# Optimization experiments

Hardware: AMD Instinct MI355X
Metric: run time of the kernel (lower is better)

The kernel has to match this reference:

```python
import jax, jax.numpy as jnp
import numpy as np

B, S, D, H = 2, 2048, 1024, 16
DH = D // H  # dim_per_head = 64


def setup_inputs() -> dict:
    key = jax.random.key(0)
    ks = jax.random.split(key, 12)
    std = 1.0 / np.sqrt(D)
    inp = {
        "key": jax.random.normal(ks[0], (B, S, D), jnp.float32),
        "value": jax.random.normal(ks[1], (B, S, D), jnp.float32),
        "query": jax.random.normal(ks[2], (B, S, D), jnp.float32),
        "mask": jax.random.randint(ks[3], (B, S, S), 0, 2) == 1,
        "Wk": jax.random.normal(ks[4], (D, D), jnp.float32) * std,
        "bk": jnp.zeros((D,), jnp.float32),
        "Wv": jax.random.normal(ks[5], (D, D), jnp.float32) * std,
        "bv": jnp.zeros((D,), jnp.float32),
        "Wq": jax.random.normal(ks[6], (D, D), jnp.float32) * std,
        "bq": jnp.zeros((D,), jnp.float32),
        "Wo": jax.random.normal(ks[7], (D, D), jnp.float32) * std,
        "bo": jnp.zeros((D,), jnp.float32),
    }
    return inp


def _shape(x):
    # (B, L, D) -> (B, H, L, DH)
    return x.reshape(B, -1, H, DH).transpose(0, 2, 1, 3)


def reference(key, value, query, mask, Wk, bk, Wv, bv, Wq, bq, Wo, bo):
    k = _shape(key @ Wk.T + bk)      # (B,H,S,DH)
    v = _shape(value @ Wv.T + bv)    # (B,H,S,DH)
    q = _shape(query @ Wq.T + bq)    # (B,H,S,DH)
    q = q / jnp.sqrt(jnp.asarray(DH, q.dtype))
    scores = jnp.einsum("bhqd,bhkd->bhqk", q, k).astype(jnp.float32)
    scores = jnp.where(mask[:, None, :, :], jnp.float32(-1e18), scores)
    attn = jax.nn.softmax(scores, axis=-1).astype(q.dtype)  # (B,H,S,S)
    # dropout p=0.0 -> identity
    ctx = jnp.einsum("bhqk,bhkd->bhqd", attn, v)
    ctx = ctx.transpose(0, 2, 1, 3).reshape(B, -1, D)
    output = ctx @ Wo.T + bo
    top_attn = attn[:, 0, :, :]
    return output, top_attn
```

## Files before the change

kernel.cpp:

```cpp
#include <hip/hip_runtime.h>

constexpr int BB = 2, SS = 2048, DD = 1024, HH = 16, DHH = 64;

typedef __attribute__((ext_vector_type(4))) float f32x4;
typedef __attribute__((ext_vector_type(8))) __bf16 bf16x8;
typedef __attribute__((ext_vector_type(8))) unsigned short us8;

__device__ __forceinline__ unsigned short f32_to_bf16(float f) {
    unsigned int u = __float_as_uint(f);
    u += 0x7fffu + ((u >> 16) & 1u);
    return (unsigned short)(u >> 16);
}

__device__ __forceinline__ ushort2 pk_bf16(float a, float b) {
#if __has_builtin(__builtin_amdgcn_cvt_pk_bf16_f32)
    typedef __attribute__((ext_vector_type(2))) __bf16 bf16x2;
    bf16x2 r = __builtin_amdgcn_cvt_pk_bf16_f32(a, b);
    return *(ushort2*)&r;
#else
    ushort2 r; r.x = f32_to_bf16(a); r.y = f32_to_bf16(b); return r;
#endif
}
__device__ __forceinline__ ushort4 pk_bf16x4(float a, float b, float c, float d) {
    const ushort2 lo = pk_bf16(a, b), hi = pk_bf16(c, d);
    ushort4 r; r.x = lo.x; r.y = lo.y; r.z = hi.x; r.w = hi.y;
    return r;
}

__device__ __forceinline__ f32x4 mfma_bf16(bf16x8 a, bf16x8 b, f32x4 c) {
    return __builtin_amdgcn_mfma_f32_16x16x32_bf16(a, b, c, 0, 0, 0);
}

__device__ __forceinline__ void stage16(const void* g, void* l) {
    typedef const __attribute__((address_space(1))) unsigned int gas_t;
    typedef __attribute__((address_space(3))) unsigned int las_t;
    __builtin_amdgcn_global_load_lds((gas_t*)(unsigned long long)g,
                                     (las_t*)(unsigned int)(unsigned long long)l,
                                     16, 0, 0);
}

__device__ __forceinline__ void cvt_block(const float* __restrict__ src,
                                          unsigned short* __restrict__ dst, int blk) {
    const size_t i = ((size_t)blk * 256 + threadIdx.x) * 8;
    const float4 a = *(const float4*)(src + i);
    const float4 b = *(const float4*)(src + i + 4);
    ushort4 lo = pk_bf16x4(a.x, a.y, a.z, a.w);
    ushort4 hi = pk_bf16x4(b.x, b.y, b.z, b.w);
    us8 o;
    o[0] = lo.x; o[1] = lo.y; o[2] = lo.z; o[3] = lo.w;
    o[4] = hi.x; o[5] = hi.y; o[6] = hi.z; o[7] = hi.w;
    *(us8*)(dst + i) = o;
}

__global__ __launch_bounds__(256) void cvt_bf16(const float* __restrict__ src,
                                                unsigned short* __restrict__ dst) {
    cvt_block(src, dst, blockIdx.x);
}

__global__ __launch_bounds__(256) void prep(const float* __restrict__ q,
                                            const float* __restrict__ k,
                                            const float* __restrict__ v,
                                            const float* __restrict__ Wq,
                                            const float* __restrict__ Wk,
                                            const float* __restrict__ Wv,
                                            unsigned short* __restrict__ Xq,
                                            unsigned short* __restrict__ Xk,
                                            unsigned short* __restrict__ Xv,
                                            unsigned short* __restrict__ Wqb,
                                            unsigned short* __restrict__ Wkb,
                                            unsigned short* __restrict__ Wvb,
                                            const int* __restrict__ mask,
                                            unsigned long long* __restrict__ pm) {
    const int id = blockIdx.x;
    if (id < 6144) {
        const int sel = id >> 11, blk = id & 2047;
        cvt_block(sel == 0 ? q : (sel == 1 ? k : v),
                  sel == 0 ? Xq : (sel == 1 ? Xk : Xv), blk);
    } else if (id < 7680) {
        const int wid = id - 6144;
        const int sel = wid >> 9, blk = wid & 511;
        cvt_block(sel == 0 ? Wq : (sel == 1 ? Wk : Wv),
                  sel == 0 ? Wqb : (sel == 1 ? Wkb : Wvb), blk);
    } else {
        const int mid = id - 7680;
        const int t = threadIdx.x, lane = t & 63;
#pragma unroll
        for (int it = 0; it < 4; ++it) {
            const size_t chunk = (size_t)mid * 16 + it * 4 + (t >> 6);
            const int val = mask[chunk * 64 + lane];
            const unsigned long long b = __ballot(val != 0);
            if (lane == 0) pm[chunk] = b;
        }
    }
}

__device__ __forceinline__ void gemm_body(int mode,
                                          const unsigned short* __restrict__ A,
                                          const unsigned short* __restrict__ Wb,
                                          const float* __restrict__ bias,
                                          void* __restrict__ outp,
                                          float scale, int nid,
                                          unsigned short* __restrict__ h0) {
    constexpr int K = DD;
    __shared__ __align__(16) unsigned short Ash[2][128][64];
    __shared__ __align__(16) unsigned short Bsh[2][64][64];

    const int n0 = (nid & 15) * 64;
    const int m0 = (nid >> 4) * 128;

    const int t = threadIdx.x;
    const int lane = t & 63, w = t >> 6;
    const int l15 = lane & 15, quad = lane >> 4;
    const int wm = (w >> 1) * 64, wn = (w & 1) * 32;

    const int srow = lane >> 3;
    const int scol8 = ((lane & 7) ^ srow) * 8;
    const unsigned short* Ag = A + (size_t)(m0 + w * 32 + srow) * K + scol8;
    const unsigned short* Bg = Wb + (size_t)(n0 + w * 16 + srow) * K + scol8;

    f32x4 acc[4][2] = {};

#pragma unroll
    for (int j = 0; j < 4; ++j) stage16(Ag + (size_t)j * 8 * K, &Ash[0][w * 32 + j * 8][0]);
#pragma unroll
    for (int j = 0; j < 2; ++j) stage16(Bg + (size_t)j * 8 * K, &Bsh[0][w * 16 + j * 8][0]);

    for (int kk = 0; kk < K / 64; ++kk) {
        const int cur = kk & 1;
        if (kk < K / 64 - 1) {
            const size_t ko = (size_t)(kk + 1) * 64;
#pragma unroll
            for (int j = 0; j < 4; ++j)
                stage16(Ag + (size_t)j * 8 * K + ko, &Ash[cur ^ 1][w * 32 + j * 8][0]);
#pragma unroll
            for (int j = 0; j < 2; ++j)
                stage16(Bg + (size_t)j * 8 * K + ko, &Bsh[cur ^ 1][w * 16 + j * 8][0]);
            __asm__ volatile("s_waitcnt vmcnt(6)" ::: "memory");
        } else {
            __asm__ volatile("s_waitcnt vmcnt(0)" ::: "memory");
        }
        __builtin_amdgcn_s_barrier();
        __builtin_amdgcn_sched_barrier(0);

        const unsigned short* Ab = &Ash[cur][0][0];
        const unsigned short* Bb = &Bsh[cur][0][0];

#pragma unroll
        for (int s = 0; s < 2; ++s) {
            const int ch = ((s * 4 + quad) ^ (l15 & 7)) * 8;
            bf16x8 af[4], bfr[2];
#pragma unroll
            for (int mi = 0; mi < 4; ++mi)
                af[mi] = *(const bf16x8*)&Ab[(wm + mi * 16 + l15) * 64 + ch];
#pragma unroll
            for (int ni = 0; ni < 2; ++ni)
                bfr[ni] = *(const bf16x8*)&Bb[(wn + ni * 16 + l15) * 64 + ch];
            __builtin_amdgcn_s_setprio(1);
#pragma unroll
            for (int mi = 0; mi < 4; ++mi)
#pragma unroll
                for (int ni = 0; ni < 2; ++ni)
                    acc[mi][ni] = mfma_bf16(af[mi], bfr[ni], acc[mi][ni]);
            __builtin_amdgcn_s_setprio(0);
        }
        __builtin_amdgcn_sched_barrier(0);
        __builtin_amdgcn_s_barrier();
        __builtin_amdgcn_sched_barrier(0);
    }

#pragma unroll
    for (int ni = 0; ni < 2; ++ni) {
        const int c = n0 + wn + ni * 16 + l15;
        const float bs = bias[c];
#pragma unroll
        for (int mi = 0; mi < 4; ++mi) {
#pragma unroll
            for (int r = 0; r < 4; ++r) {
                const int mrow = m0 + wm + mi * 16 + quad * 4 + r;
                const float val = (acc[mi][ni][r] + bs) * scale;
                if (mode == 2) {
                    ((float*)outp)[(size_t)mrow * DD + c] = val;
                } else {
                    const int bi2 = mrow >> 11, si = mrow & (SS - 1);
                    const int hi2 = c >> 6, di = c & (DHH - 1);
                    unsigned short* o = (unsigned short*)outp;
                    const unsigned short v16 = f32_to_bf16(val);
                    if (mode == 0) {
                        o[((size_t)(bi2 * HH + hi2) * SS + si) * DHH + di] = v16;
                        if (h0 != nullptr && hi2 == 0)
                            h0[((size_t)bi2 * SS + si) * DHH + di] = v16;
                    } else {
                        o[((size_t)(bi2 * HH + hi2) * DHH + di) * SS + si] = v16;
                    }
                }
            }
        }
    }
}

__global__ __launch_bounds__(256) void gemm_qv(const unsigned short* __restrict__ Xq,
                                               const unsigned short* __restrict__ Wqb,
                                               const float* __restrict__ bq,
                                               unsigned short* __restrict__ qws,
                                               float qscale,
                                               unsigned short* __restrict__ q0,
                                               const unsigned short* __restrict__ Xv,
                                               const unsigned short* __restrict__ Wvb,
                                               const float* __restrict__ bv,
                                               unsigned short* __restrict__ vws) {
    const int id = blockIdx.x;
    const int gid = id >> 9, id9 = id & 511;
    const int nid = (id9 & 7) * 64 + (id9 >> 3);
    gemm_body(gid, gid ? Xv : Xq, gid ? Wvb : Wqb, gid ? bv : bq,
              gid ? (void*)vws : (void*)qws, gid ? 1.0f : qscale, nid,
              gid ? nullptr : q0);
}

template <int MODE>
__global__ __launch_bounds__(256) void gemm_one(const unsigned short* __restrict__ A,
                                                const unsigned short* __restrict__ Wb,
                                                const float* __restrict__ bias,
                                                void* __restrict__ outp,
                                                float scale,
                                                unsigned short* __restrict__ h0) {
    const int id = blockIdx.x;
    const int nid = (id & 7) * 64 + (id >> 3);
    gemm_body(MODE, A, Wb, bias, outp, scale, nid, h0);
}

__global__ __launch_bounds__(512, 4) void flash_attn(const unsigned short* __restrict__ qws,
                                                     const unsigned short* __restrict__ kws,
                                                     const unsigned short* __restrict__ vws,
                                                     const unsigned long long* __restrict__ pm,
                                                     unsigned short* __restrict__ ctx,
                                                     float2* __restrict__ stats) {
    __shared__ __align__(16) unsigned short Ksh[2][64][64];
    __shared__ __align__(16) unsigned short Vsh[2][64][64];
    __shared__ __align__(16) unsigned short Psh[8][16][72];

    constexpr int NQT = SS / 128;
    const int id = blockIdx.x;
    const int nid = (id & 7) * 64 + (id >> 3);
    const int qt = nid % NQT;
    const int bh = nid / NQT;
    const int bi = bh / HH, hi = bh % HH;

    const int t = threadIdx.x;
    const int lane = t & 63, w = t >> 6;
    const int l15 = lane & 15, quad = lane >> 4;
    const int sh4 = quad * 4;
    const int xk = quad ^ (l15 & 7);

    const unsigned short* qp = qws + (size_t)bh * SS * DHH;
    const unsigned short* kp = kws + (size_t)bh * SS * DHH;
    const unsigned short* vp = vws + (size_t)bh * DHH * SS;

    const int q_loc = qt * 128 + w * 16 + l15;
    const bf16x8 bq0 = *(const bf16x8*)(qp + (size_t)q_loc * DHH + quad * 8);
    const bf16x8 bq1 = *(const bf16x8*)(qp + (size_t)q_loc * DHH + 32 + quad * 8);
    const unsigned long long* pmrow = pm + ((size_t)bi * SS + q_loc) * (SS / 64);

    const int srow = lane >> 3;
    const int scol = (lane & 7) ^ srow;
    const unsigned short* kg = kp + (size_t)(w * 8 + srow) * DHH + scol * 8;
    const unsigned short* vg = vp + (size_t)(w * 8 + srow) * SS + scol * 8;

    f32x4 accO[4] = {};
    float m_run = -1e30f, l_run = 0.f;
    const float NEG_INF = -__builtin_inff();

    unsigned long long mcur = pmrow[0];
    stage16(kg, &Ksh[0][w * 8][0]);
    stage16(vg, &Vsh[0][w * 8][0]);

    constexpr int NT = SS / 64;
    for (int kt = 0; kt < NT; ++kt) {
        const int cur = kt & 1;
        unsigned long long mnxt = 0;
        if (kt < NT - 1) {
            mnxt = pmrow[kt + 1];
            stage16(kg + (size_t)(kt + 1) * 64 * DHH, &Ksh[cur ^ 1][w * 8][0]);
            stage16(vg + (size_t)(kt + 1) * 64,       &Vsh[cur ^ 1][w * 8][0]);
            __asm__ volatile("s_waitcnt vmcnt(3)" ::: "memory");
        } else {
            __asm__ volatile("s_waitcnt vmcnt(0)" ::: "memory");
        }
        __builtin_amdgcn_s_barrier();
        __builtin_amdgcn_sched_barrier(0);

        const unsigned short* Kb = &Ksh[cur][0][0];
        const unsigned short* Vb = &Vsh[cur][0][0];

        bf16x8 ak0[4], ak1[4];
#pragma unroll
        for (int i = 0; i < 4; ++i) {
            ak0[i] = *(const bf16x8*)&Kb[(i * 16 + l15) * 64 + xk * 8];
            ak1[i] = *(const bf16x8*)&Kb[(i * 16 + l15) * 64 + (xk ^ 4) * 8];
        }

        const unsigned int mlo = ((unsigned int)mcur) >> sh4;
        const unsigned int mhi = ((unsigned int)(mcur >> 32)) >> sh4;

        float sc[4][4];
        __builtin_amdgcn_s_setprio(1);
#pragma unroll
        for (int i = 0; i < 4; ++i) {
            f32x4 s4 = {};
            s4 = mfma_bf16(ak0[i], bq0, s4);
            s4 = mfma_bf16(ak1[i], bq1, s4);
            const unsigned int mw = (i & 2) ? mhi : mlo;
#pragma unroll
            for (int r = 0; r < 4; ++r)
                sc[i][r] = ((mw >> ((i & 1) * 16 + r)) & 1u) ? NEG_INF : s4[r];
        }
        __builtin_amdgcn_s_setprio(0);

        bf16x8 av0[4], av1[4];
#pragma unroll
        for (int i = 0; i < 4; ++i) {
            av0[i] = *(const bf16x8*)&Vb[(i * 16 + l15) * 64 + xk * 8];
            av1[i] = *(const bf16x8*)&Vb[(i * 16 + l15) * 64 + (xk ^ 4) * 8];
        }

        float tm = sc[0][0];
#pragma unroll
        for (int i = 0; i < 4; ++i)
#pragma unroll
            for (int r = 0; r < 4; ++r) tm = fmaxf(tm, sc[i][r]);
        tm = fmaxf(tm, __shfl_xor(tm, 16));
        tm = fmaxf(tm, __shfl_xor(tm, 32));

        const bool nodefer = !__all(tm <= m_run + 8.0f);
        const float mn = nodefer ? fmaxf(m_run, tm) : m_run;

        float rs = 0.f;
#pragma unroll
        for (int i = 0; i < 4; ++i)
#pragma unroll
            for (int r = 0; r < 4; ++r) {
                const float p = __builtin_amdgcn_exp2f(sc[i][r] - mn);
                sc[i][r] = p;
                rs += p;
            }
        rs += __shfl_xor(rs, 16);
        rs += __shfl_xor(rs, 32);

        if (nodefer) {
            const float alpha = __builtin_amdgcn_exp2f(m_run - mn);
            l_run = l_run * alpha + rs;
            m_run = mn;
#pragma unroll
            for (int i = 0; i < 4; ++i) accO[i] *= alpha;
        } else {
            l_run += rs;
        }

#pragma unroll
        for (int i = 0; i < 4; ++i)
            *(ushort4*)&Psh[w][l15][i * 16 + sh4] =
                pk_bf16x4(sc[i][0], sc[i][1], sc[i][2], sc[i][3]);
        __asm__ volatile("s_waitcnt lgkmcnt(0)" ::: "memory");

        const bf16x8 p0 = *(const bf16x8*)&Psh[w][l15][quad * 8];
        const bf16x8 p1 = *(const bf16x8*)&Psh[w][l15][32 + quad * 8];
        __builtin_amdgcn_s_setprio(1);
#pragma unroll
        for (int i = 0; i < 4; ++i) {
            accO[i] = mfma_bf16(av0[i], p0, accO[i]);
            accO[i] = mfma_bf16(av1[i], p1, accO[i]);
        }
        __builtin_amdgcn_s_setprio(0);

        __builtin_amdgcn_sched_barrier(0);
        __builtin_amdgcn_s_barrier();
        __builtin_amdgcn_sched_barrier(0);
        mcur = mnxt;
    }

    const float inv = 1.0f / l_run;
    unsigned short* cb = ctx + ((size_t)(bi * SS) + q_loc) * DD + hi * DHH;
#pragma unroll
    for (int i = 0; i < 4; ++i)
        *(ushort4*)&cb[i * 16 + sh4] = pk_bf16x4(accO[i][0] * inv, accO[i][1] * inv,
                                                 accO[i][2] * inv, accO[i][3] * inv);

    if (hi == 0 && quad == 0) {
        float2 st; st.x = m_run; st.y = l_run;
        stats[(size_t)bi * SS + q_loc] = st;
    }
}

__global__ __launch_bounds__(256) void prob_h0(const unsigned short* __restrict__ q0,
                                               const unsigned short* __restrict__ k0,
                                               const unsigned long long* __restrict__ pm,
                                               const float2* __restrict__ stats,
                                               float* __restrict__ outp) {
    __shared__ __align__(16) unsigned short Ksh[64][72];

    const int id = blockIdx.x;
    const int nid = (id & 7) * 64 + (id >> 3);
    const int kc = nid & 7;
    const int qt = (nid >> 3) & 31;
    const int bi = nid >> 8;

    const int t = threadIdx.x;
    const int lane = t & 63, w = t >> 6;
    const int l15 = lane & 15, quad = lane >> 4;
    const int sh4 = quad * 4;

    const int q = qt * 64 + w * 16 + l15;
    const unsigned short* qp = q0 + ((size_t)bi * SS + q) * DHH;
    const bf16x8 bq0 = *(const bf16x8*)(qp + quad * 8);
    const bf16x8 bq1 = *(const bf16x8*)(qp + 32 + quad * 8);

    const unsigned short* kp = k0 + (size_t)bi * SS * DHH;
    const unsigned long long* pmq = pm + ((size_t)bi * SS + q) * (SS / 64);
    float* orow = outp + ((size_t)bi * SS + q) * SS;

    const float2 st = stats[(size_t)bi * SS + q];
    const float M = st.x;
    const float invL = 1.0f / st.y;

    for (int kt = 0; kt < 4; ++kt) {
        const int key0 = kc * 256 + kt * 64;
        __syncthreads();
#pragma unroll
        for (int hf = 0; hf < 2; ++hf) {
            const int v = t + hf * 256;
            const int row = v >> 3, off = (v & 7) * 8;
            *(us8*)&Ksh[row][off] = *(const us8*)(kp + (size_t)(key0 + row) * DHH + off);
        }
        __syncthreads();

        const unsigned long long m64 = pmq[kc * 4 + kt];
        const unsigned int mlo = ((unsigned int)m64) >> sh4;
        const unsigned int mhi = ((unsigned int)(m64 >> 32)) >> sh4;

#pragma unroll
        for (int i = 0; i < 4; ++i) {
            const bf16x8 ak0 = *(const bf16x8*)&Ksh[i * 16 + l15][quad * 8];
            const bf16x8 ak1 = *(const bf16x8*)&Ksh[i * 16 + l15][32 + quad * 8];
            f32x4 s4 = {};
            s4 = mfma_bf16(ak0, bq0, s4);
            s4 = mfma_bf16(ak1, bq1, s4);
            const unsigned int mw = (i & 2) ? mhi : mlo;
            float4 ov;
#pragma unroll
            for (int r = 0; r < 4; ++r) {
                const float p = __builtin_amdgcn_exp2f(s4[r] - M) * invL;
                ((float*)&ov)[r] = ((mw >> ((i & 1) * 16 + r)) & 1u) ? 0.0f : p;
            }
            *(float4*)&orow[key0 + i * 16 + sh4] = ov;
        }
    }
}

extern "C" void kernel_launch(void* const* d_in, const int* in_sizes, int n_in,
                              void* d_out, int out_size, void* d_ws, size_t ws_size,
                              hipStream_t stream) {
    const float* key_   = (const float*)d_in[0];
    const float* value_ = (const float*)d_in[1];
    const float* query_ = (const float*)d_in[2];
    const int*   mask_  = (const int*)d_in[3];
    const float* Wk = (const float*)d_in[4];
    const float* bk = (const float*)d_in[5];
    const float* Wv = (const float*)d_in[6];
    const float* bv = (const float*)d_in[7];
    const float* Wq = (const float*)d_in[8];
    const float* bq = (const float*)d_in[9];
    const float* Wo = (const float*)d_in[10];
    const float* bo = (const float*)d_in[11];

    constexpr size_t XS  = (size_t)BB * SS * DD;
    constexpr size_t WSZ = (size_t)DD * DD;

    float* out_f = (float*)d_out;
    unsigned short* scratch = (unsigned short*)(out_f + XS);
    unsigned short* qws = scratch;
    unsigned short* kws = qws + XS;
    unsigned short* vws = kws + XS;
    unsigned short* ctx = vws + XS;

    unsigned short* q0 = (unsigned short*)d_ws;
    unsigned short* k0 = q0 + (size_t)BB * SS * DHH;
    unsigned long long* pm = (unsigned long long*)(k0 + (size_t)BB * SS * DHH);
    float2* stats = (float2*)(pm + (size_t)BB * SS * (SS / 64));

    unsigned short* Xq  = (unsigned short*)out_f;
    unsigned short* Xk  = Xq + XS;
    unsigned short* Xv  = kws;
    unsigned short* Wqb = ctx;
    unsigned short* Wkb = Wqb + WSZ;
    unsigned short* Wvb = Wkb + WSZ;
    unsigned short* Wob = qws;

    const float qscale = 0.125f * 1.4426950408889634f;

    prep<<<15872, 256, 0, stream>>>(query_, key_, value_, Wq, Wk, Wv,
                                    Xq, Xk, Xv, Wqb, Wkb, Wvb, mask_, pm);

    gemm_qv<<<1024, 256, 0, stream>>>(Xq, Wqb, bq, qws, qscale, q0,
                                      Xv, Wvb, bv, vws);

    gemm_one<0><<<512, 256, 0, stream>>>(Xk, Wkb, bk, kws, 1.0f, k0);

    flash_attn<<<BB * HH * (SS / 128), 512, 0, stream>>>(qws, kws, vws, pm, ctx, stats);

    cvt_bf16<<<WSZ / 2048, 256, 0, stream>>>(Wo, Wob);

    gemm_one<2><<<512, 256, 0, stream>>>(ctx, Wob, bo, out_f, 1.0f, nullptr);

    prob_h0<<<512, 256, 0, stream>>>(q0, k0, pm, stats, out_f + XS);
}
```

Measured before the change: 302.9 us.

## Fuse Q/K/V projections into one 128x128-tile GEMM, fusing V fp32 conversion

Replaces the separate Q+V and K projection launches with one gemm_qkv kernel that uses 512-thread blocks and 128x128 output tiles. The V path reads fp32 value directly, converts it to bf16 in registers and writes it into swizzled LDS, so V no longer needs a pre-conversion pass in prep. The transposed V output is staged through LDS so it can be written with vectorized stores. The output projection also moves to a 128x128 tile with 512 threads, which halves the block count and increases reuse per block, at the cost of fewer blocks to fill the GPU.

```diff
diff --git a/kernel.cpp b/kernel.cpp
--- a/kernel.cpp
+++ b/kernel.cpp
@@ -26,6 +26,14 @@
     ushort4 r; r.x = lo.x; r.y = lo.y; r.z = hi.x; r.w = hi.y;
     return r;
 }
+__device__ __forceinline__ us8 cvt_us8(float4 a, float4 b) {
+    const ushort4 lo = pk_bf16x4(a.x, a.y, a.z, a.w);
+    const ushort4 hi = pk_bf16x4(b.x, b.y, b.z, b.w);
+    us8 o;
+    o[0] = lo.x; o[1] = lo.y; o[2] = lo.z; o[3] = lo.w;
+    o[4] = hi.x; o[5] = hi.y; o[6] = hi.z; o[7] = hi.w;
+    return o;
+}
 
 __device__ __forceinline__ f32x4 mfma_bf16(bf16x8 a, bf16x8 b, f32x4 c) {
     return __builtin_amdgcn_mfma_f32_16x16x32_bf16(a, b, c, 0, 0, 0);
@@ -44,12 +52,7 @@
     const size_t i = ((size_t)blk * 256 + threadIdx.x) * 8;
     const float4 a = *(const float4*)(src + i);
     const float4 b = *(const float4*)(src + i + 4);
-    ushort4 lo = pk_bf16x4(a.x, a.y, a.z, a.w);
-    ushort4 hi = pk_bf16x4(b.x, b.y, b.z, b.w);
-    us8 o;
-    o[0] = lo.x; o[1] = lo.y; o[2] = lo.z; o[3] = lo.w;
-    o[4] = hi.x; o[5] = hi.y; o[6] = hi.z; o[7] = hi.w;
-    *(us8*)(dst + i) = o;
+    *(us8*)(dst + i) = cvt_us8(a, b);
 }
 
 __global__ __launch_bounds__(256) void cvt_bf16(const float* __restrict__ src,
@@ -59,30 +62,27 @@
 
 __global__ __launch_bounds__(256) void prep(const float* __restrict__ q,
                                             const float* __restrict__ k,
-                                            const float* __restrict__ v,
                                             const float* __restrict__ Wq,
                                             const float* __restrict__ Wk,
                                             const float* __restrict__ Wv,
                                             unsigned short* __restrict__ Xq,
                                             unsigned short* __restrict__ Xk,
-                                            unsigned short* __restrict__ Xv,
                                             unsigned short* __restrict__ Wqb,
                                             unsigned short* __restrict__ Wkb,
                                             unsigned short* __restrict__ Wvb,
                                             const int* __restrict__ mask,
                                             unsigned long long* __restrict__ pm) {
     const int id = blockIdx.x;
-    if (id < 6144) {
+    if (id < 4096) {
         const int sel = id >> 11, blk = id & 2047;
-        cvt_block(sel == 0 ? q : (sel == 1 ? k : v),
-                  sel == 0 ? Xq : (sel == 1 ? Xk : Xv), blk);
-    } else if (id < 7680) {
-        const int wid = id - 6144;
+        cvt_block(sel == 0 ? q : k, sel == 0 ? Xq : Xk, blk);
+    } else if (id < 5632) {
+        const int wid = id - 4096;
         const int sel = wid >> 9, blk = wid & 511;
         cvt_block(sel == 0 ? Wq : (sel == 1 ? Wk : Wv),
                   sel == 0 ? Wqb : (sel == 1 ? Wkb : Wvb), blk);
     } else {
-        const int mid = id - 7680;
+        const int mid = id - 5632;
         const int t = threadIdx.x, lane = t & 63;
 #pragma unroll
         for (int it = 0; it < 4; ++it) {
@@ -94,56 +94,99 @@
     }
 }
 
-__device__ __forceinline__ void gemm_body(int mode,
-                                          const unsigned short* __restrict__ A,
-                                          const unsigned short* __restrict__ Wb,
-                                          const float* __restrict__ bias,
-                                          void* __restrict__ outp,
-                                          float scale, int nid,
-                                          unsigned short* __restrict__ h0) {
+__global__ __launch_bounds__(512) void gemm_qkv(
+    const unsigned short* __restrict__ Xq, const unsigned short* __restrict__ Xk,
+    const float* __restrict__ Vf,
+    const unsigned short* __restrict__ Wqb, const unsigned short* __restrict__ Wkb,
+    const unsigned short* __restrict__ Wvb,
+    const float* __restrict__ bq, const float* __restrict__ bk,
+    const float* __restrict__ bv,
+    unsigned short* __restrict__ qws, unsigned short* __restrict__ kws,
+    unsigned short* __restrict__ vws,
+    unsigned short* __restrict__ q0, unsigned short* __restrict__ k0,
+    float qscale) {
     constexpr int K = DD;
-    __shared__ __align__(16) unsigned short Ash[2][128][64];
-    __shared__ __align__(16) unsigned short Bsh[2][64][64];
-
-    const int n0 = (nid & 15) * 64;
-    const int m0 = (nid >> 4) * 128;
+    __shared__ __align__(16) unsigned short AB[2][2][128][64];
+
+    const int id = blockIdx.x;
+    const int nid = (id & 7) * 96 + (id >> 3);
+    const int which = nid >> 8;
+    const int r8 = nid & 255;
+    const int m0 = (r8 >> 3) * 128;
+    const int n0 = (r8 & 7) * 128;
 
     const int t = threadIdx.x;
     const int lane = t & 63, w = t >> 6;
     const int l15 = lane & 15, quad = lane >> 4;
-    const int wm = (w >> 1) * 64, wn = (w & 1) * 32;
+    const int wm = (w >> 2) * 64, wn = (w & 3) * 32;
+    const bool vp = (which == 2);
+
+    const unsigned short* Ab = which == 0 ? Xq : Xk;
+    const unsigned short* Wb = which == 0 ? Wqb : (which == 1 ? Wkb : Wvb);
+    const float* bias = which == 0 ? bq : (which == 1 ? bk : bv);
+    const float scale = which == 0 ? qscale : 1.0f;
 
     const int srow = lane >> 3;
     const int scol8 = ((lane & 7) ^ srow) * 8;
-    const unsigned short* Ag = A + (size_t)(m0 + w * 32 + srow) * K + scol8;
-    const unsigned short* Bg = Wb + (size_t)(n0 + w * 16 + srow) * K + scol8;
+    const unsigned short* Agp = Ab + (size_t)(m0 + w * 8 + srow) * K + scol8;
+    const unsigned short* Bgp = Wb + (size_t)(n0 + w * 8 + srow) * K + scol8;
+
+    const int vrow = t >> 3, vc = t & 7;
+    const float* Vg = Vf + (size_t)(m0 + vrow) * K + vc * 8;
 
     f32x4 acc[4][2] = {};
-
-#pragma unroll
-    for (int j = 0; j < 4; ++j) stage16(Ag + (size_t)j * 8 * K, &Ash[0][w * 32 + j * 8][0]);
-#pragma unroll
-    for (int j = 0; j < 2; ++j) stage16(Bg + (size_t)j * 8 * K, &Bsh[0][w * 16 + j * 8][0]);
+    float4 va0, va1, va2, va3;
+
+    if (!vp) {
+#pragma unroll
+        for (int j = 0; j < 2; ++j) {
+            stage16(Agp + (size_t)(j * 64) * K, &AB[0][0][w * 8 + j * 64][0]);
+            stage16(Bgp + (size_t)(j * 64) * K, &AB[1][0][w * 8 + j * 64][0]);
+        }
+    } else {
+        va0 = *(const float4*)(Vg);
+        va1 = *(const float4*)(Vg + 4);
+        va2 = *(const float4*)(Vg + (size_t)64 * K);
+        va3 = *(const float4*)(Vg + (size_t)64 * K + 4);
+#pragma unroll
+        for (int j = 0; j < 2; ++j)
+            stage16(Bgp + (size_t)(j * 64) * K, &AB[1][0][w * 8 + j * 64][0]);
+        {
+            const int wr0 = vrow, wr1 = 64 + vrow;
+            *(us8*)((unsigned char*)&AB[0][0][0][0] + wr0 * 128 + ((vc ^ (wr0 & 7)) * 16))
+                = cvt_us8(va0, va1);
+            *(us8*)((unsigned char*)&AB[0][0][0][0] + wr1 * 128 + ((vc ^ (wr1 & 7)) * 16))
+                = cvt_us8(va2, va3);
+        }
+        __asm__ volatile("s_waitcnt lgkmcnt(0)" ::: "memory");
+    }
 
     for (int kk = 0; kk < K / 64; ++kk) {
         const int cur = kk & 1;
         if (kk < K / 64 - 1) {
             const size_t ko = (size_t)(kk + 1) * 64;
-#pragma unroll
-            for (int j = 0; j < 4; ++j)
-                stage16(Ag + (size_t)j * 8 * K + ko, &Ash[cur ^ 1][w * 32 + j * 8][0]);
-#pragma unroll
-            for (int j = 0; j < 2; ++j)
-                stage16(Bg + (size_t)j * 8 * K + ko, &Bsh[cur ^ 1][w * 16 + j * 8][0]);
-            __asm__ volatile("s_waitcnt vmcnt(6)" ::: "memory");
+            if (!vp) {
+#pragma unroll
+                for (int j = 0; j < 2; ++j) {
+                    stage16(Agp + (size_t)(j * 64) * K + ko, &AB[0][cur ^ 1][w * 8 + j * 64][0]);
+                    stage16(Bgp + (size_t)(j * 64) * K + ko, &AB[1][cur ^ 1][w * 8 + j * 64][0]);
+                }
+                __asm__ volatile("s_waitcnt vmcnt(4)" ::: "memory");
+            } else {
+                va0 = *(const float4*)(Vg + ko);
+                va1 = *(const float4*)(Vg + ko + 4);
+                va2 = *(const float4*)(Vg + (size_t)64 * K + ko);
+                va3 = *(const float4*)(Vg + (size_t)64 * K + ko + 4);
+#pragma unroll
+                for (int j = 0; j < 2; ++j)
+                    stage16(Bgp + (size_t)(j * 64) * K + ko, &AB[1][cur ^ 1][w * 8 + j * 64][0]);
+                __asm__ volatile("s_waitcnt vmcnt(6)" ::: "memory");
+            }
         } else {
             __asm__ volatile("s_waitcnt vmcnt(0)" ::: "memory");
         }
         __builtin_amdgcn_s_barrier();
         __builtin_amdgcn_sched_barrier(0);
-
-        const unsigned short* Ab = &Ash[cur][0][0];
-        const unsigned short* Bb = &Bsh[cur][0][0];
 
 #pragma unroll
         for (int s = 0; s < 2; ++s) {
@@ -151,10 +194,10 @@
             bf16x8 af[4], bfr[2];
 #pragma unroll
             for (int mi = 0; mi < 4; ++mi)
-                af[mi] = *(const bf16x8*)&Ab[(wm + mi * 16 + l15) * 64 + ch];
+                af[mi] = *(const bf16x8*)&AB[0][cur][wm + mi * 16 + l15][ch];
 #pragma unroll
             for (int ni = 0; ni < 2; ++ni)
-                bfr[ni] = *(const bf16x8*)&Bb[(wn + ni * 16 + l15) * 64 + ch];
+                bfr[ni] = *(const bf16x8*)&AB[1][cur][wn + ni * 16 + l15][ch];
             __builtin_amdgcn_s_setprio(1);
 #pragma unroll
             for (int mi = 0; mi < 4; ++mi)
@@ -163,6 +206,133 @@
                     acc[mi][ni] = mfma_bf16(af[mi], bfr[ni], acc[mi][ni]);
             __builtin_amdgcn_s_setprio(0);
         }
+
+        if (vp && kk < K / 64 - 1) {
+            const int wr0 = vrow, wr1 = 64 + vrow;
+            *(us8*)((unsigned char*)&AB[0][cur ^ 1][0][0] + wr0 * 128 + ((vc ^ (wr0 & 7)) * 16))
+                = cvt_us8(va0, va1);
+            *(us8*)((unsigned char*)&AB[0][cur ^ 1][0][0] + wr1 * 128 + ((vc ^ (wr1 & 7)) * 16))
+                = cvt_us8(va2, va3);
+            __asm__ volatile("s_waitcnt lgkmcnt(0)" ::: "memory");
+        }
+
+        __builtin_amdgcn_sched_barrier(0);
+        __builtin_amdgcn_s_barrier();
+        __builtin_amdgcn_sched_barrier(0);
+    }
+
+    if (which < 2) {
+        unsigned short* o = which == 0 ? qws : kws;
+        unsigned short* h0 = which == 0 ? q0 : k0;
+#pragma unroll
+        for (int ni = 0; ni < 2; ++ni) {
+            const int c = n0 + wn + ni * 16 + l15;
+            const float bs = bias[c];
+            const int hi2 = c >> 6, di = c & (DHH - 1);
+#pragma unroll
+            for (int mi = 0; mi < 4; ++mi) {
+#pragma unroll
+                for (int r = 0; r < 4; ++r) {
+                    const int mrow = m0 + wm + mi * 16 + quad * 4 + r;
+                    const int bi2 = mrow >> 11, si = mrow & (SS - 1);
+                    const unsigned short v16 = f32_to_bf16((acc[mi][ni][r] + bs) * scale);
+                    o[((size_t)(bi2 * HH + hi2) * SS + si) * DHH + di] = v16;
+                    if (hi2 == 0)
+                        h0[((size_t)bi2 * SS + si) * DHH + di] = v16;
+                }
+            }
+        }
+    } else {
+        unsigned short* scr = (unsigned short*)&AB[0][0][0][0] + w * (32 * 72);
+#pragma unroll
+        for (int ni = 0; ni < 2; ++ni) {
+            const int c = n0 + wn + ni * 16 + l15;
+            const float bs = bias[c];
+#pragma unroll
+            for (int mi = 0; mi < 4; ++mi)
+                *(ushort4*)&scr[(ni * 16 + l15) * 72 + mi * 16 + quad * 4] =
+                    pk_bf16x4(acc[mi][ni][0] + bs, acc[mi][ni][1] + bs,
+                              acc[mi][ni][2] + bs, acc[mi][ni][3] + bs);
+        }
+        __asm__ volatile("s_waitcnt lgkmcnt(0)" ::: "memory");
+        const int mb = m0 + wm;
+        const int bi2 = mb >> 11, si0 = mb & (SS - 1);
+        const int rowc = lane & 7;
+#pragma unroll
+        for (int k2 = 0; k2 < 4; ++k2) {
+            const int col = k2 * 8 + (lane >> 3);
+            const us8 vv = *(const us8*)&scr[col * 72 + rowc * 8];
+            const int c = n0 + wn + col;
+            *(us8*)&vws[((size_t)(bi2 * HH + (c >> 6)) * DHH + (c & 63)) * SS
+                        + si0 + rowc * 8] = vv;
+        }
+    }
+}
+
+__global__ __launch_bounds__(512) void gemm_o(const unsigned short* __restrict__ A,
+                                              const unsigned short* __restrict__ Wb,
+                                              const float* __restrict__ bias,
+                                              float* __restrict__ outp) {
+    constexpr int K = DD;
+    __shared__ __align__(16) unsigned short AB[2][2][128][64];
+
+    const int id = blockIdx.x;
+    const int nid = (id & 7) * 32 + (id >> 3);
+    const int m0 = (nid >> 3) * 128;
+    const int n0 = (nid & 7) * 128;
+
+    const int t = threadIdx.x;
+    const int lane = t & 63, w = t >> 6;
+    const int l15 = lane & 15, quad = lane >> 4;
+    const int wm = (w >> 2) * 64, wn = (w & 3) * 32;
+
+    const int srow = lane >> 3;
+    const int scol8 = ((lane & 7) ^ srow) * 8;
+    const unsigned short* Agp = A + (size_t)(m0 + w * 8 + srow) * K + scol8;
+    const unsigned short* Bgp = Wb + (size_t)(n0 + w * 8 + srow) * K + scol8;
+
+    f32x4 acc[4][2] = {};
+
+#pragma unroll
+    for (int j = 0; j < 2; ++j) {
+        stage16(Agp + (size_t)(j * 64) * K, &AB[0][0][w * 8 + j * 64][0]);
+        stage16(Bgp + (size_t)(j * 64) * K, &AB[1][0][w * 8 + j * 64][0]);
+    }
+
+    for (int kk = 0; kk < K / 64; ++kk) {
+        const int cur = kk & 1;
+        if (kk < K / 64 - 1) {
+            const size_t ko = (size_t)(kk + 1) * 64;
+#pragma unroll
+            for (int j = 0; j < 2; ++j) {
+                stage16(Agp + (size_t)(j * 64) * K + ko, &AB[0][cur ^ 1][w * 8 + j * 64][0]);
+                stage16(Bgp + (size_t)(j * 64) * K + ko, &AB[1][cur ^ 1][w * 8 + j * 64][0]);
+            }
+            __asm__ volatile("s_waitcnt vmcnt(4)" ::: "memory");
+        } else {
+            __asm__ volatile("s_waitcnt vmcnt(0)" ::: "memory");
+        }
+        __builtin_amdgcn_s_barrier();
+        __builtin_amdgcn_sched_barrier(0);
+
+#pragma unroll
+        for (int s = 0; s < 2; ++s) {
+            const int ch = ((s * 4 + quad) ^ (l15 & 7)) * 8;
+            bf16x8 af[4], bfr[2];
+#pragma unroll
+            for (int mi = 0; mi < 4; ++mi)
+                af[mi] = *(const bf16x8*)&AB[0][cur][wm + mi * 16 + l15][ch];
+#pragma unroll
+            for (int ni = 0; ni < 2; ++ni)
+                bfr[ni] = *(const bf16x8*)&AB[1][cur][wn + ni * 16 + l15][ch];
+            __builtin_amdgcn_s_setprio(1);
+#pragma unroll
+            for (int mi = 0; mi < 4; ++mi)
+#pragma unroll
+                for (int ni = 0; ni < 2; ++ni)
+                    acc[mi][ni] = mfma_bf16(af[mi], bfr[ni], acc[mi][ni]);
+            __builtin_amdgcn_s_setprio(0);
+        }
         __builtin_amdgcn_sched_barrier(0);
         __builtin_amdgcn_s_barrier();
         __builtin_amdgcn_sched_barrier(0);
@@ -173,59 +343,13 @@
         const int c = n0 + wn + ni * 16 + l15;
         const float bs = bias[c];
 #pragma unroll
-        for (int mi = 0; mi < 4; ++mi) {
+        for (int mi = 0; mi < 4; ++mi)
 #pragma unroll
             for (int r = 0; r < 4; ++r) {
                 const int mrow = m0 + wm + mi * 16 + quad * 4 + r;
-                const float val = (acc[mi][ni][r] + bs) * scale;
-                if (mode == 2) {
-                    ((float*)outp)[(size_t)mrow * DD + c] = val;
-                } else {
-                    const int bi2 = mrow >> 11, si = mrow & (SS - 1);
-                    const int hi2 = c >> 6, di = c & (DHH - 1);
-                    unsigned short* o = (unsigned short*)outp;
-                    const unsigned short v16 = f32_to_bf16(val);
-                    if (mode == 0) {
-                        o[((size_t)(bi2 * HH + hi2) * SS + si) * DHH + di] = v16;
-                        if (h0 != nullptr && hi2 == 0)
-                            h0[((size_t)bi2 * SS + si) * DHH + di] = v16;
-                    } else {
-                        o[((size_t)(bi2 * HH + hi2) * DHH + di) * SS + si] = v16;
-                    }
-                }
+                outp[(size_t)mrow * DD + c] = acc[mi][ni][r] + bs;
             }
-        }
-    }
-}
-
-__global__ __launch_bounds__(256) void gemm_qv(const unsigned short* __restrict__ Xq,
-                                               const unsigned short* __restrict__ Wqb,
-                                               const float* __restrict__ bq,
-                                               unsigned short* __restrict__ qws,
-                                               float qscale,
-                                               unsigned short* __restrict__ q0,
-                                               const unsigned short* __restrict__ Xv,
-                                               const unsigned short* __restrict__ Wvb,
-                                               const float* __restrict__ bv,
-                                               unsigned short* __restrict__ vws) {
-    const int id = blockIdx.x;
-    const int gid = id >> 9, id9 = id & 511;
-    const int nid = (id9 & 7) * 64 + (id9 >> 3);
-    gemm_body(gid, gid ? Xv : Xq, gid ? Wvb : Wqb, gid ? bv : bq,
-              gid ? (void*)vws : (void*)qws, gid ? 1.0f : qscale, nid,
-              gid ? nullptr : q0);
-}
-
-template <int MODE>
-__global__ __launch_bounds__(256) void gemm_one(const unsigned short* __restrict__ A,
-                                                const unsigned short* __restrict__ Wb,
-                                                const float* __restrict__ bias,
-                                                void* __restrict__ outp,
-                                                float scale,
-                                                unsigned short* __restrict__ h0) {
-    const int id = blockIdx.x;
-    const int nid = (id & 7) * 64 + (id >> 3);
-    gemm_body(MODE, A, Wb, bias, outp, scale, nid, h0);
+    }
 }
 
 __global__ __launch_bounds__(512, 4) void flash_attn(const unsigned short* __restrict__ qws,
@@ -488,7 +612,6 @@
 
     unsigned short* Xq  = (unsigned short*)out_f;
     unsigned short* Xk  = Xq + XS;
-    unsigned short* Xv  = kws;
     unsigned short* Wqb = ctx;
     unsigned short* Wkb = Wqb + WSZ;
     unsigned short* Wvb = Wkb + WSZ;
@@ -496,19 +619,17 @@
 
     const float qscale = 0.125f * 1.4426950408889634f;
 
-    prep<<<15872, 256, 0, stream>>>(query_, key_, value_, Wq, Wk, Wv,
-                                    Xq, Xk, Xv, Wqb, Wkb, Wvb, mask_, pm);
-
-    gemm_qv<<<1024, 256, 0, stream>>>(Xq, Wqb, bq, qws, qscale, q0,
-                                      Xv, Wvb, bv, vws);
-
-    gemm_one<0><<<512, 256, 0, stream>>>(Xk, Wkb, bk, kws, 1.0f, k0);
+    prep<<<13824, 256, 0, stream>>>(query_, key_, Wq, Wk, Wv,
+                                    Xq, Xk, Wqb, Wkb, Wvb, mask_, pm);
+
+    gemm_qkv<<<768, 512, 0, stream>>>(Xq, Xk, value_, Wqb, Wkb, Wvb,
+                                      bq, bk, bv, qws, kws, vws, q0, k0, qscale);
 
     flash_attn<<<BB * HH * (SS / 128), 512, 0, stream>>>(qws, kws, vws, pm, ctx, stats);
 
     cvt_bf16<<<WSZ / 2048, 256, 0, stream>>>(Wo, Wob);
 
-    gemm_one<2><<<512, 256, 0, stream>>>(ctx, Wob, bo, out_f, 1.0f, nullptr);
+    gemm_o<<<256, 512, 0, stream>>>(ctx, Wob, bo, out_f);
 
     prob_h0<<<512, 256, 0, stream>>>(q0, k0, pm, stats, out_f + XS);
 }
```

Result: no change. 308.9 us (+2.0%).
